# Performance work log

Measured on AMD Instinct MI355X. Metric: run time of the kernel, lower is better.

Reference implementation:

```python
import jax, jax.numpy as jnp
import numpy as np

NUM_GRAPHS = 64
NEG_SLOPE = 0.2


def gat_layer(x, src, dst, W, a_src, a_dst, b, concat):
    # x: [N, F_in], W: [F_in, H*C], a_src/a_dst: [H, C], b: [H*C] or [C]
    N = x.shape[0]
    H, C = a_src.shape
    h = (x @ W).reshape(N, H, C)                      # [N, H, C]
    alpha_src = jnp.sum(h * a_src[None], axis=-1)     # [N, H]
    alpha_dst = jnp.sum(h * a_dst[None], axis=-1)     # [N, H]
    e = alpha_src[src] + alpha_dst[dst]               # [E, H]
    e = jax.nn.leaky_relu(e, NEG_SLOPE)
    # segment softmax over incoming edges of each dst node
    m = jax.ops.segment_max(e, dst, num_segments=N)   # [N, H]
    ex = jnp.exp(e - m[dst])
    s = jax.ops.segment_sum(ex, dst, num_segments=N)  # [N, H]
    alpha = ex / (s[dst] + 1e-16)                     # [E, H]
    msg = h[src] * alpha[:, :, None]                  # [E, H, C]
    out = jax.ops.segment_sum(msg, dst, num_segments=N)  # [N, H, C]
    if concat:
        out = out.reshape(N, H * C)
    else:
        out = out.mean(axis=1)
    return out + b


def setup_inputs() -> dict:
    key = jax.random.key(0)
    ks = jax.random.split(key, 12)
    N, E, F_in, Hd, Out, H = 50000, 400000, 128, 64, 64, 8
    x = jax.random.normal(ks[0], (N, F_in), dtype=jnp.float32)
    edge_index = jax.random.randint(ks[1], (2, E), 0, N, dtype=jnp.int64)
    batch = jnp.sort(jax.random.randint(ks[2], (N,), 0, NUM_GRAPHS, dtype=jnp.int64))
    s1 = 1.0 / np.sqrt(F_in)
    W1 = jax.random.normal(ks[3], (F_in, H * Hd), dtype=jnp.float32) * s1
    a_src1 = jax.random.normal(ks[4], (H, Hd), dtype=jnp.float32) * 0.1
    a_dst1 = jax.random.normal(ks[5], (H, Hd), dtype=jnp.float32) * 0.1
    b1 = jnp.zeros((H * Hd,), dtype=jnp.float32)
    s2 = 1.0 / np.sqrt(H * Hd)
    W2 = jax.random.normal(ks[6], (H * Hd, H * Out), dtype=jnp.float32) * s2
    a_src2 = jax.random.normal(ks[7], (H, Out), dtype=jnp.float32) * 0.1
    a_dst2 = jax.random.normal(ks[8], (H, Out), dtype=jnp.float32) * 0.1
    b2 = jnp.zeros((Out,), dtype=jnp.float32)
    return {"x": x, "edge_index": edge_index, "batch": batch,
            "W1": W1, "a_src1": a_src1, "a_dst1": a_dst1, "b1": b1,
            "W2": W2, "a_src2": a_src2, "a_dst2": a_dst2, "b2": b2}


def reference(x, edge_index, batch, W1, a_src1, a_dst1, b1, W2, a_src2, a_dst2, b2):
    N = x.shape[0]
    # add self-loops (PyG GATConv default add_self_loops=True)
    loop = jnp.arange(N, dtype=edge_index.dtype)
    src = jnp.concatenate([edge_index[0], loop])
    dst = jnp.concatenate([edge_index[1], loop])
    h = jax.nn.elu(gat_layer(x, src, dst, W1, a_src1, a_dst1, b1, concat=True))
    h = jax.nn.elu(gat_layer(h, src, dst, W2, a_src2, a_dst2, b2, concat=False))
    # global mean pool over graphs
    sums = jax.ops.segment_sum(h, batch, num_segments=NUM_GRAPHS)
    cnts = jax.ops.segment_sum(jnp.ones((N,), h.dtype), batch, num_segments=NUM_GRAPHS)
    return sums / jnp.maximum(cnts, 1.0)[:, None]
```

## Files before the change

### kernel.cpp

```cpp
#include <hip/hip_runtime.h>
#include <hip/hip_bf16.h>
#include <hip/hip_fp16.h>
#include <math.h>

#define NN   50000
#define NE   400000
#define NET  450000
#define FH   8
#define FC   64
#define FHC  512
#define FIN  128
#define NG   64
#define MPAD 50048
#define NB   196

typedef unsigned short u16;
typedef _Float16 f16x8 __attribute__((ext_vector_type(8)));
typedef float f32x4 __attribute__((ext_vector_type(4)));
typedef unsigned short u16x8 __attribute__((ext_vector_type(8)));

static __device__ __forceinline__ u16 f2h(float f) {
  return __half_as_ushort(__float2half(f));
}
static __device__ __forceinline__ float h2f(u16 u) {
  return __half2float(__ushort_as_half(u));
}

__global__ __launch_bounds__(256) void conv_h_k(const float* __restrict__ in,
                                                u16* __restrict__ outp,
                                                int n4) {
  int t = blockIdx.x * 256 + threadIdx.x;
  if (t >= n4) return;
  float4 f = reinterpret_cast<const float4*>(in)[t];
  ushort4 h;
  h.x = f2h(f.x); h.y = f2h(f.y); h.z = f2h(f.z); h.w = f2h(f.w);
  reinterpret_cast<ushort4*>(outp)[t] = h;
}

__global__ __launch_bounds__(256) void conv_wt_k(const float* __restrict__ W,
                                                 u16* __restrict__ hT,
                                                 int K) {
  int t = blockIdx.x * 256 + threadIdx.x;
  if (t >= K * FHC) return;
  int k = t >> 9, n = t & 511;
  hT[n * K + k] = f2h(W[t]);
}

__global__ __launch_bounds__(256) void gemm_mfma(const u16* __restrict__ Af,
                                                 const u16* __restrict__ Bf,
                                                 u16* __restrict__ Cb,
                                                 const float* __restrict__ As_g,
                                                 const float* __restrict__ Ad_g,
                                                 float* __restrict__ asrc,
                                                 float* __restrict__ adst,
                                                 int M, int K) {
  constexpr int BK = 64;
  __shared__ u16 As[128 * BK];
  __shared__ u16 Bs[128 * BK];
  const int tid = threadIdx.x;
  constexpr int NWG = (MPAD / 128) * (FHC / 128);
  constexpr int qq = NWG >> 3, rr = NWG & 7;
  int d = blockIdx.x;
  int xcd = d & 7, slot = d >> 3;
  int w = (xcd < rr) ? xcd * (qq + 1) + slot
                     : rr * (qq + 1) + (xcd - rr) * qq + slot;
  const int bm = (w >> 2) * 128;
  const int bn = (w & 3) * 128;
  const int wv = tid >> 6, l = tid & 63;
  const int wr = wv >> 1, wc = wv & 1;
  const int fr = l & 15, fq = l >> 4;

  f32x4 acc[4][4] = {};

  for (int k0 = 0; k0 < K; k0 += BK) {
    __syncthreads();
#pragma unroll
    for (int i = 0; i < 4; ++i) {
      int idx = i * 256 + tid;
      int row = idx >> 3, c8 = idx & 7;
      size_t goA = (size_t)(bm + row) * K + k0 + c8 * 8;
      size_t goB = (size_t)(bn + row) * K + k0 + c8 * 8;
      __builtin_amdgcn_global_load_lds(
          (const __attribute__((address_space(1))) void*)(Af + goA),
          (__attribute__((address_space(3))) void*)(As + idx * 8), 16, 0, 0);
      __builtin_amdgcn_global_load_lds(
          (const __attribute__((address_space(1))) void*)(Bf + goB),
          (__attribute__((address_space(3))) void*)(Bs + idx * 8), 16, 0, 0);
    }
    __syncthreads();
#pragma unroll
    for (int kk = 0; kk < 2; ++kk) {
      f16x8 av[4], bv[4];
#pragma unroll
      for (int mi = 0; mi < 4; ++mi)
        av[mi] = *reinterpret_cast<const f16x8*>(
            As + (wr * 64 + mi * 16 + fr) * BK + kk * 32 + fq * 8);
#pragma unroll
      for (int ni = 0; ni < 4; ++ni)
        bv[ni] = *reinterpret_cast<const f16x8*>(
            Bs + (wc * 64 + ni * 16 + fr) * BK + kk * 32 + fq * 8);
#pragma unroll
      for (int mi = 0; mi < 4; ++mi)
#pragma unroll
        for (int ni = 0; ni < 4; ++ni)
          acc[mi][ni] = __builtin_amdgcn_mfma_f32_16x16x32_f16(
              av[mi], bv[ni], acc[mi][ni], 0, 0, 0);
    }
  }
#pragma unroll
  for (int mi = 0; mi < 4; ++mi)
#pragma unroll
    for (int ni = 0; ni < 4; ++ni) {
      int r0 = bm + wr * 64 + mi * 16 + fq * 4;
      int c0 = bn + wc * 64 + ni * 16 + fr;
#pragma unroll
      for (int j = 0; j < 4; ++j)
        if (r0 + j < M) Cb[(size_t)(r0 + j) * FHC + c0] = f2h(acc[mi][ni][j]);
    }
  {
    int hd = (bn >> 6) + wc;
    int cb = bn + wc * 64 + fr;
    float as_v[4], ad_v[4];
#pragma unroll
    for (int ni = 0; ni < 4; ++ni) {
      as_v[ni] = As_g[cb + ni * 16];
      ad_v[ni] = Ad_g[cb + ni * 16];
    }
#pragma unroll
    for (int mi = 0; mi < 4; ++mi)
#pragma unroll
      for (int j = 0; j < 4; ++j) {
        float ps = 0.f, pd = 0.f;
#pragma unroll
        for (int ni = 0; ni < 4; ++ni) {
          float v = acc[mi][ni][j];
          ps += v * as_v[ni];
          pd += v * ad_v[ni];
        }
#pragma unroll
        for (int off = 1; off < 16; off <<= 1) {
          ps += __shfl_xor(ps, off);
          pd += __shfl_xor(pd, off);
        }
        int row = bm + wr * 64 + mi * 16 + fq * 4 + j;
        if (fr == 0 && row < M) {
          asrc[row * FH + hd] = ps;
          adst[row * FH + hd] = pd;
        }
      }
  }
}

__global__ __launch_bounds__(256) void hist_k(const int* __restrict__ ei,
                                              int* __restrict__ deg) {
  int e = blockIdx.x * 256 + threadIdx.x;
  if (e >= NET) return;
  int d = (e < NE) ? ei[NE + e] : e - NE;
  atomicAdd(&deg[d], 1);
}

__global__ __launch_bounds__(256) void scan1_k(const int* __restrict__ deg,
                                               int* __restrict__ row_ptr,
                                               int* __restrict__ bsum) {
  int tid = threadIdx.x;
  int i = blockIdx.x * 256 + tid;
  int lane = tid & 63, w = tid >> 6;
  int val = (i < NN) ? deg[i] : 0;
  int s = val;
#pragma unroll
  for (int off = 1; off < 64; off <<= 1) {
    int t = __shfl_up(s, off);
    if (lane >= off) s += t;
  }
  __shared__ int wt[4], wo[4];
  if (lane == 63) wt[w] = s;
  __syncthreads();
  if (tid == 0) {
    int r = 0;
#pragma unroll
    for (int k = 0; k < 4; ++k) { wo[k] = r; r += wt[k]; }
    bsum[blockIdx.x] = r;
  }
  __syncthreads();
  if (i < NN) row_ptr[i] = s - val + wo[w];
}

__global__ __launch_bounds__(256) void scan2_k(int* __restrict__ bsum,
                                               int* __restrict__ row_ptr) {
  int tid = threadIdx.x;
  int lane = tid & 63, w = tid >> 6;
  int val = (tid < NB) ? bsum[tid] : 0;
  int s = val;
#pragma unroll
  for (int off = 1; off < 64; off <<= 1) {
    int t = __shfl_up(s, off);
    if (lane >= off) s += t;
  }
  __shared__ int wt[4], wo[4];
  if (lane == 63) wt[w] = s;
  __syncthreads();
  if (tid == 0) {
    int r = 0;
#pragma unroll
    for (int k = 0; k < 4; ++k) { wo[k] = r; r += wt[k]; }
  }
  __syncthreads();
  int excl = s - val + wo[w];
  if (tid < NB) bsum[tid] = excl;
  if (tid == 255) row_ptr[NN] = excl;
}

__global__ __launch_bounds__(256) void scan3_k(int* __restrict__ row_ptr,
                                               const int* __restrict__ bsum,
                                               int* __restrict__ cursor) {
  int i = blockIdx.x * 256 + threadIdx.x;
  if (i >= NN) return;
  int v = row_ptr[i] + bsum[blockIdx.x];
  row_ptr[i] = v;
  cursor[i] = v;
}

__global__ __launch_bounds__(256) void fill_k(const int* __restrict__ ei,
                                              int* __restrict__ cursor,
                                              int* __restrict__ col_src) {
  int e = blockIdx.x * 256 + threadIdx.x;
  if (e >= NET) return;
  int s, d;
  if (e < NE) { s = ei[e]; d = ei[NE + e]; } else { s = d = e - NE; }
  int pos = atomicAdd(&cursor[d], 1);
  col_src[pos] = s;
}

__global__ __launch_bounds__(256) void bnd_k(const int* __restrict__ batch,
                                             int* __restrict__ gstart,
                                             int* __restrict__ gend) {
  int n = blockIdx.x * 256 + threadIdx.x;
  if (n >= NN) return;
  int b = batch[n];
  if (n == 0 || batch[n - 1] != b) gstart[b] = n;
  if (n == NN - 1 || batch[n + 1] != b) gend[b] = n + 1;
}

template <int LAYER>
__global__ __launch_bounds__(256) void gather_k(const int* __restrict__ row_ptr,
                                                const int* __restrict__ col_src,
                                                const float* __restrict__ asrc,
                                                const float* __restrict__ adst,
                                                const u16* __restrict__ hb,
                                                const float* __restrict__ bias,
                                                u16* __restrict__ outb,
                                                float* __restrict__ nodeval) {
  int n = blockIdx.x * 4 + (threadIdx.x >> 6);
  if (n >= NN) return;
  int lane = threadIdx.x & 63;
  int hh = lane & 7;
  int hsel = lane >> 3;
  int start = row_ptr[n], end = row_ptr[n + 1];
  float adn = adst[n * FH + hh];
  float den = 0.f;
  float v[8] = {};
  for (int j0 = start; j0 < end; j0 += 4) {
    int sidx[4];
#pragma unroll
    for (int u = 0; u < 4; ++u) {
      int jj = (j0 + u < end) ? j0 + u : end - 1;
      sidx[u] = col_src[jj];
    }
    float ex[4];
#pragma unroll
    for (int u = 0; u < 4; ++u) {
      float el = asrc[sidx[u] * FH + hh] + adn;
      el = el > 0.f ? el : 0.2f * el;
      ex[u] = (j0 + u < end) ? __expf(el) : 0.f;
      den += ex[u];
    }
    u16x8 hv[4];
#pragma unroll
    for (int u = 0; u < 4; ++u)
      hv[u] = *reinterpret_cast<const u16x8*>(hb + (size_t)sidx[u] * FHC + lane * 8);
#pragma unroll
    for (int u = 0; u < 4; ++u) {
      float exv = __shfl(ex[u], hsel);
#pragma unroll
      for (int j = 0; j < 8; ++j) v[j] += exv * h2f(hv[u][j]);
    }
  }
  float dh = __shfl(den, hsel);
  float inv = 1.f / (dh + 1e-16f);
#pragma unroll
  for (int j = 0; j < 8; ++j) v[j] *= inv;
  if (LAYER == 1) {
    const float4* bp = reinterpret_cast<const float4*>(bias + lane * 8);
    float4 b0 = bp[0], b1 = bp[1];
    float bb[8] = {b0.x, b0.y, b0.z, b0.w, b1.x, b1.y, b1.z, b1.w};
    u16x8 ov;
#pragma unroll
    for (int j = 0; j < 8; ++j) {
      float val = v[j] + bb[j];
      val = val > 0.f ? val : expm1f(val);
      ov[j] = f2h(val);
    }
    *reinterpret_cast<u16x8*>(outb + (size_t)n * FHC + lane * 8) = ov;
  } else {
#pragma unroll
    for (int off = 8; off < 64; off <<= 1)
#pragma unroll
      for (int j = 0; j < 8; ++j) v[j] += __shfl_xor(v[j], off);
    if (lane < 8) {
      const float4* bp = reinterpret_cast<const float4*>(bias + lane * 8);
      float4 b0 = bp[0], b1 = bp[1];
      float bb[8] = {b0.x, b0.y, b0.z, b0.w, b1.x, b1.y, b1.z, b1.w};
      float o[8];
#pragma unroll
      for (int j = 0; j < 8; ++j) {
        float val = v[j] * (1.f / FH) + bb[j];
        o[j] = val > 0.f ? val : expm1f(val);
      }
      float4* np = reinterpret_cast<float4*>(nodeval + (size_t)n * FC + lane * 8);
      np[0] = make_float4(o[0], o[1], o[2], o[3]);
      np[1] = make_float4(o[4], o[5], o[6], o[7]);
    }
  }
}

__global__ __launch_bounds__(256) void pool_k(const float* __restrict__ nodeval,
                                              const int* __restrict__ gstart,
                                              const int* __restrict__ gend,
                                              float* __restrict__ out) {
  __shared__ float red[4][FC];
  int g = blockIdx.x;
  int c = threadIdx.x & 63, w = threadIdx.x >> 6;
  int s = gstart[g], e = gend[g];
  float acc = 0.f;
  for (int n = s + w; n < e; n += 4) acc += nodeval[(size_t)n * FC + c];
  red[w][c] = acc;
  __syncthreads();
  if (w == 0) {
    float v = red[0][c] + red[1][c] + red[2][c] + red[3][c];
    out[g * FC + c] = v / fmaxf((float)(e - s), 1.f);
  }
}

extern "C" void kernel_launch(void* const* d_in, const int* in_sizes, int n_in,
                              void* d_out, int out_size, void* d_ws, size_t ws_size,
                              hipStream_t stream) {
  const float* x    = (const float*)d_in[0];
  const int*   ei   = (const int*)d_in[1];
  const int*   batch= (const int*)d_in[2];
  const float* W1   = (const float*)d_in[3];
  const float* as1  = (const float*)d_in[4];
  const float* ad1  = (const float*)d_in[5];
  const float* b1   = (const float*)d_in[6];
  const float* W2   = (const float*)d_in[7];
  const float* as2  = (const float*)d_in[8];
  const float* ad2  = (const float*)d_in[9];
  const float* b2   = (const float*)d_in[10];
  float* out = (float*)d_out;

  char* p = (char*)d_ws;
  u16* Cb  = (u16*)p; p += (size_t)NN * FHC * 2;
  u16* xf  = (u16*)p; p += (size_t)MPAD * FIN * 2;
  u16* h1f = (u16*)p; p += (size_t)MPAD * FHC * 2;
  u16* w1t = (u16*)p; p += (size_t)FHC * FIN * 2;
  u16* w2t = (u16*)p; p += (size_t)FHC * FHC * 2;
  float* asrc = (float*)p;            p += (size_t)NN * FH * 4;
  float* adst = (float*)p;            p += (size_t)NN * FH * 4;
  int* deg    = (int*)p;              p += (size_t)NN * 4;
  int* rowp   = (int*)p;              p += (size_t)(NN + 1) * 4;
  int* cursor = (int*)p;              p += (size_t)NN * 4;
  int* col    = (int*)p;              p += (size_t)NET * 4;
  int* gstart = (int*)p;              p += (size_t)NG * 4;
  int* gend   = (int*)p;              p += (size_t)NG * 4;
  int* bsum   = (int*)p;              p += (size_t)NB * 4;
  float* nodeval = (float*)xf;

  const int NWG = (MPAD / 128) * (FHC / 128);
  const int egrid = (NET + 255) / 256;
  const int ngrid = (NN + 3) / 4;

  hipMemsetAsync(deg, 0, (size_t)NN * 4, stream);
  hipMemsetAsync(gstart, 0, (size_t)NG * 2 * 4, stream);
  hipMemsetAsync(xf + (size_t)NN * FIN, 0, (size_t)(MPAD - NN) * FIN * 2, stream);
  hipMemsetAsync(h1f + (size_t)NN * FHC, 0, (size_t)(MPAD - NN) * FHC * 2, stream);

  conv_h_k<<<(NN * FIN / 4 + 255) / 256, 256, 0, stream>>>(x, xf, NN * FIN / 4);
  conv_wt_k<<<(FIN * FHC + 255) / 256, 256, 0, stream>>>(W1, w1t, FIN);
  conv_wt_k<<<(FHC * FHC + 255) / 256, 256, 0, stream>>>(W2, w2t, FHC);

  hist_k<<<egrid, 256, 0, stream>>>(ei, deg);
  scan1_k<<<NB, 256, 0, stream>>>(deg, rowp, bsum);
  scan2_k<<<1, 256, 0, stream>>>(bsum, rowp);
  scan3_k<<<NB, 256, 0, stream>>>(rowp, bsum, cursor);
  fill_k<<<egrid, 256, 0, stream>>>(ei, cursor, col);
  bnd_k<<<(NN + 255) / 256, 256, 0, stream>>>(batch, gstart, gend);

  gemm_mfma<<<NWG, 256, 0, stream>>>(xf, w1t, Cb, as1, ad1, asrc, adst, NN, FIN);
  gather_k<1><<<ngrid, 256, 0, stream>>>(rowp, col, asrc, adst, Cb, b1,
                                         h1f, nullptr);

  gemm_mfma<<<NWG, 256, 0, stream>>>(h1f, w2t, Cb, as2, ad2, asrc, adst, NN, FHC);
  gather_k<2><<<ngrid, 256, 0, stream>>>(rowp, col, asrc, adst, Cb, b2,
                                         nullptr, nodeval);

  pool_k<<<NG, 256, 0, stream>>>(nodeval, gstart, gend, out);
}
```

Measured before the change: 383.0 us.

## Fuse prep conversions and memsets into one kernel, merge fill/bnd, halve GEMM BK

Replaces four memsets and three conversion kernels with a single prep kernel that converts x, transposes W1/W2 to fp16 and zeroes the padding, degree and graph-boundary buffers. Merges the CSR fill and graph-boundary kernels into one launch. Separately reduces the GEMM K-tile from 64 to 32, which halves LDS use and may raise occupancy, at the cost of twice as many sync-separated load iterations.

```diff
diff --git a/kernel.cpp b/kernel.cpp
--- a/kernel.cpp
+++ b/kernel.cpp
@@ -26,24 +26,61 @@
   return __half2float(__ushort_as_half(u));
 }
 
-__global__ __launch_bounds__(256) void conv_h_k(const float* __restrict__ in,
-                                                u16* __restrict__ outp,
-                                                int n4) {
+#define R0 (NN * FIN / 4)
+#define R1 (FIN * FHC)
+#define R2 (FHC * FHC)
+#define R3 ((MPAD - NN) * FIN / 8)
+#define R4 ((MPAD - NN) * FHC / 8)
+#define R5 (NN / 4)
+#define R6 (2 * NG)
+#define PREP_T (R0 + R1 + R2 + R3 + R4 + R5 + R6)
+
+__global__ __launch_bounds__(256) void prep_k(const float* __restrict__ x,
+                                              const float* __restrict__ W1,
+                                              const float* __restrict__ W2,
+                                              u16* __restrict__ xf,
+                                              u16* __restrict__ w1t,
+                                              u16* __restrict__ w2t,
+                                              u16* __restrict__ h1f,
+                                              int* __restrict__ deg,
+                                              int* __restrict__ gse) {
   int t = blockIdx.x * 256 + threadIdx.x;
-  if (t >= n4) return;
-  float4 f = reinterpret_cast<const float4*>(in)[t];
-  ushort4 h;
-  h.x = f2h(f.x); h.y = f2h(f.y); h.z = f2h(f.z); h.w = f2h(f.w);
-  reinterpret_cast<ushort4*>(outp)[t] = h;
-}
-
-__global__ __launch_bounds__(256) void conv_wt_k(const float* __restrict__ W,
-                                                 u16* __restrict__ hT,
-                                                 int K) {
-  int t = blockIdx.x * 256 + threadIdx.x;
-  if (t >= K * FHC) return;
-  int k = t >> 9, n = t & 511;
-  hT[n * K + k] = f2h(W[t]);
+  if (t < R0) {
+    float4 f = reinterpret_cast<const float4*>(x)[t];
+    ushort4 h;
+    h.x = f2h(f.x); h.y = f2h(f.y); h.z = f2h(f.z); h.w = f2h(f.w);
+    reinterpret_cast<ushort4*>(xf)[t] = h;
+    return;
+  }
+  t -= R0;
+  if (t < R1) {
+    int k = t >> 9, n = t & 511;
+    w1t[n * FIN + k] = f2h(W1[t]);
+    return;
+  }
+  t -= R1;
+  if (t < R2) {
+    int k = t >> 9, n = t & 511;
+    w2t[n * FHC + k] = f2h(W2[t]);
+    return;
+  }
+  t -= R2;
+  if (t < R3) {
+    reinterpret_cast<u16x8*>(xf + (size_t)NN * FIN)[t] = (u16x8)0;
+    return;
+  }
+  t -= R3;
+  if (t < R4) {
+    reinterpret_cast<u16x8*>(h1f + (size_t)NN * FHC)[t] = (u16x8)0;
+    return;
+  }
+  t -= R4;
+  if (t < R5) {
+    reinterpret_cast<int4*>(deg)[t] = make_int4(0, 0, 0, 0);
+    return;
+  }
+  t -= R5;
+  if (t < R6) gse[t] = 0;
 }
 
 __global__ __launch_bounds__(256) void gemm_mfma(const u16* __restrict__ Af,
@@ -54,7 +91,7 @@
                                                  float* __restrict__ asrc,
                                                  float* __restrict__ adst,
                                                  int M, int K) {
-  constexpr int BK = 64;
+  constexpr int BK = 32;
   __shared__ u16 As[128 * BK];
   __shared__ u16 Bs[128 * BK];
   const int tid = threadIdx.x;
@@ -75,9 +112,9 @@
   for (int k0 = 0; k0 < K; k0 += BK) {
     __syncthreads();
 #pragma unroll
-    for (int i = 0; i < 4; ++i) {
+    for (int i = 0; i < 2; ++i) {
       int idx = i * 256 + tid;
-      int row = idx >> 3, c8 = idx & 7;
+      int row = idx >> 2, c8 = idx & 3;
       size_t goA = (size_t)(bm + row) * K + k0 + c8 * 8;
       size_t goB = (size_t)(bn + row) * K + k0 + c8 * 8;
       __builtin_amdgcn_global_load_lds(
@@ -88,17 +125,16 @@
           (__attribute__((address_space(3))) void*)(Bs + idx * 8), 16, 0, 0);
     }
     __syncthreads();
-#pragma unroll
-    for (int kk = 0; kk < 2; ++kk) {
+    {
       f16x8 av[4], bv[4];
 #pragma unroll
       for (int mi = 0; mi < 4; ++mi)
         av[mi] = *reinterpret_cast<const f16x8*>(
-            As + (wr * 64 + mi * 16 + fr) * BK + kk * 32 + fq * 8);
+            As + (wr * 64 + mi * 16 + fr) * BK + fq * 8);
 #pragma unroll
       for (int ni = 0; ni < 4; ++ni)
         bv[ni] = *reinterpret_cast<const f16x8*>(
-            Bs + (wc * 64 + ni * 16 + fr) * BK + kk * 32 + fq * 8);
+            Bs + (wc * 64 + ni * 16 + fr) * BK + fq * 8);
 #pragma unroll
       for (int mi = 0; mi < 4; ++mi)
 #pragma unroll
@@ -220,21 +256,21 @@
   cursor[i] = v;
 }
 
-__global__ __launch_bounds__(256) void fill_k(const int* __restrict__ ei,
-                                              int* __restrict__ cursor,
-                                              int* __restrict__ col_src) {
-  int e = blockIdx.x * 256 + threadIdx.x;
-  if (e >= NET) return;
-  int s, d;
-  if (e < NE) { s = ei[e]; d = ei[NE + e]; } else { s = d = e - NE; }
-  int pos = atomicAdd(&cursor[d], 1);
-  col_src[pos] = s;
-}
-
-__global__ __launch_bounds__(256) void bnd_k(const int* __restrict__ batch,
-                                             int* __restrict__ gstart,
-                                             int* __restrict__ gend) {
-  int n = blockIdx.x * 256 + threadIdx.x;
+__global__ __launch_bounds__(256) void fillbnd_k(const int* __restrict__ ei,
+                                                 int* __restrict__ cursor,
+                                                 int* __restrict__ col_src,
+                                                 const int* __restrict__ batch,
+                                                 int* __restrict__ gstart,
+                                                 int* __restrict__ gend) {
+  int t = blockIdx.x * 256 + threadIdx.x;
+  if (t < NET) {
+    int s, d;
+    if (t < NE) { s = ei[t]; d = ei[NE + t]; } else { s = d = t - NE; }
+    int pos = atomicAdd(&cursor[d], 1);
+    col_src[pos] = s;
+    return;
+  }
+  int n = t - NET;
   if (n >= NN) return;
   int b = batch[n];
   if (n == 0 || batch[n - 1] != b) gstart[b] = n;
@@ -369,30 +405,24 @@
   int* rowp   = (int*)p;              p += (size_t)(NN + 1) * 4;
   int* cursor = (int*)p;              p += (size_t)NN * 4;
   int* col    = (int*)p;              p += (size_t)NET * 4;
-  int* gstart = (int*)p;              p += (size_t)NG * 4;
-  int* gend   = (int*)p;              p += (size_t)NG * 4;
+  int* gse    = (int*)p;              p += (size_t)NG * 2 * 4;
   int* bsum   = (int*)p;              p += (size_t)NB * 4;
+  int* gstart = gse;
+  int* gend   = gse + NG;
   float* nodeval = (float*)xf;
 
   const int NWG = (MPAD / 128) * (FHC / 128);
-  const int egrid = (NET + 255) / 256;
   const int ngrid = (NN + 3) / 4;
 
-  hipMemsetAsync(deg, 0, (size_t)NN * 4, stream);
-  hipMemsetAsync(gstart, 0, (size_t)NG * 2 * 4, stream);
-  hipMemsetAsync(xf + (size_t)NN * FIN, 0, (size_t)(MPAD - NN) * FIN * 2, stream);
-  hipMemsetAsync(h1f + (size_t)NN * FHC, 0, (size_t)(MPAD - NN) * FHC * 2, stream);
-
-  conv_h_k<<<(NN * FIN / 4 + 255) / 256, 256, 0, stream>>>(x, xf, NN * FIN / 4);
-  conv_wt_k<<<(FIN * FHC + 255) / 256, 256, 0, stream>>>(W1, w1t, FIN);
-  conv_wt_k<<<(FHC * FHC + 255) / 256, 256, 0, stream>>>(W2, w2t, FHC);
-
-  hist_k<<<egrid, 256, 0, stream>>>(ei, deg);
+  prep_k<<<(PREP_T + 255) / 256, 256, 0, stream>>>(x, W1, W2, xf, w1t, w2t,
+                                                   h1f, deg, gse);
+
+  hist_k<<<(NET + 255) / 256, 256, 0, stream>>>(ei, deg);
   scan1_k<<<NB, 256, 0, stream>>>(deg, rowp, bsum);
   scan2_k<<<1, 256, 0, stream>>>(bsum, rowp);
   scan3_k<<<NB, 256, 0, stream>>>(rowp, bsum, cursor);
-  fill_k<<<egrid, 256, 0, stream>>>(ei, cursor, col);
-  bnd_k<<<(NN + 255) / 256, 256, 0, stream>>>(batch, gstart, gend);
+  fillbnd_k<<<(NET + NN + 255) / 256, 256, 0, stream>>>(ei, cursor, col,
+                                                        batch, gstart, gend);
 
   gemm_mfma<<<NWG, 256, 0, stream>>>(xf, w1t, Cb, as1, ad1, asrc, adst, NN, FIN);
   gather_k<1><<<ngrid, 256, 0, stream>>>(rowp, col, asrc, adst, Cb, b1,
```

After: 348.6 us. 9.0% less time.
